# Performance work log

Measured on AMD Instinct MI355X. Metric: run time of the kernel, lower is better.

The kernel has to match this reference:

```python
import jax, jax.numpy as jnp
import numpy as np

DIM = 128
N = 4096


def setup_inputs() -> dict:
    key = jax.random.key(0)
    ks = jax.random.split(key, 12)
    d = DIM
    s = 0.02
    inp = jax.random.normal(ks[0], (N, 2 * d), dtype=jnp.float32)
    # H = myLinear: (2d -> 5d -> 1), tanh after each layer
    Hw1 = jax.random.normal(ks[1], (2 * d, 5 * d), dtype=jnp.float32) * s
    Hb1 = jax.random.normal(ks[2], (5 * d,), dtype=jnp.float32) * s
    Hw2 = jax.random.normal(ks[3], (5 * d, 1), dtype=jnp.float32) * s
    Hb2 = jax.random.normal(ks[4], (1,), dtype=jnp.float32) * s
    # augment_f: (d -> 4d -> 8d -> d*d), tanh after each layer
    Aw1 = jax.random.normal(ks[5], (d, 4 * d), dtype=jnp.float32) * s
    Ab1 = jax.random.normal(ks[6], (4 * d,), dtype=jnp.float32) * s
    Aw2 = jax.random.normal(ks[7], (4 * d, 8 * d), dtype=jnp.float32) * s
    Ab2 = jax.random.normal(ks[8], (8 * d,), dtype=jnp.float32) * s
    Aw3 = jax.random.normal(ks[9], (8 * d, d * d), dtype=jnp.float32) * s
    Ab3 = jax.random.normal(ks[10], (d * d,), dtype=jnp.float32) * s
    u = jax.random.uniform(ks[11], (d,), dtype=jnp.float32, minval=-0.001, maxval=0.001)
    return {"t": 0, "inp": inp, "Hw1": Hw1, "Hb1": Hb1, "Hw2": Hw2, "Hb2": Hb2,
            "Aw1": Aw1, "Ab1": Ab1, "Aw2": Aw2, "Ab2": Ab2, "Aw3": Aw3, "Ab3": Ab3, "u": u}


def reference(t, inp, Hw1, Hb1, Hw2, Hb2, Aw1, Ab1, Aw2, Ab2, Aw3, Ab3, u):
    d = DIM
    n = inp.shape[0]

    def H_scalar(z):  # z: [2d] -> scalar
        h = jnp.tanh(z @ Hw1 + Hb1)
        return jnp.tanh(h @ Hw2 + Hb2)[0]

    # per-sample gradient of scalar H w.r.t. input (== batch_jacobian squeeze)
    g = jax.vmap(jax.grad(H_scalar))(inp)  # [N, 2d]
    dx = g[:, :d]
    dv = -g[:, d:]

    x = inp[:, :d]
    h1 = jnp.tanh(x @ Aw1 + Ab1)            # [N, 4d]
    h2 = jnp.tanh(h1 @ Aw2 + Ab2)           # [N, 8d]
    gq = jnp.tanh(h2 @ Aw3 + Ab3).reshape(n, d, d)  # [N, d, d]
    dv = dv + jnp.einsum("nij,j->ni", gq, u)
    return jnp.concatenate([dx, dv], axis=-1)  # [N, 2d]
```

## Files before the change

### kernel.cpp

```cpp
#include <hip/hip_runtime.h>
#include <hip/hip_bf16.h>
#include <cstdint>


typedef __bf16 bf16_t;
typedef __bf16 bf16x4_t __attribute__((ext_vector_type(4)));
typedef __bf16 bf16x8_t __attribute__((ext_vector_type(8)));
typedef float f32x4_t __attribute__((ext_vector_type(4)));
typedef float f32x16_t __attribute__((ext_vector_type(16)));
typedef int intx4_t __attribute__((ext_vector_type(4)));
typedef int intx8_t __attribute__((ext_vector_type(8)));

#define DIMD 128
#define NROW 4096
#define SMEM_G64 24576
#define SMEM3_BYTES 24576

__device__ __forceinline__ float fast_tanh(float x) {
  float t = __builtin_amdgcn_exp2f(x * 2.8853900817779268f);
  return 1.f - 2.f * __builtin_amdgcn_rcpf(t + 1.f);
}

__device__ __forceinline__ uint8_t to_fp8(float x) {
  return (uint8_t)(__builtin_amdgcn_cvt_pk_fp8_f32(x, x, 0, false) & 0xff);
}

__device__ __forceinline__ uint32_t pk4_fp8(float a, float b, float c,
                                            float d) {
  uint32_t lo = (uint32_t)__builtin_amdgcn_cvt_pk_fp8_f32(a, b, 0, false);
  return (uint32_t)__builtin_amdgcn_cvt_pk_fp8_f32(c, d, lo, true);
}

__device__ __forceinline__ void g2l16(const void* gp, void* lp) {
  __builtin_amdgcn_global_load_lds(
      reinterpret_cast<__attribute__((address_space(1))) void*>(
          reinterpret_cast<uintptr_t>(gp)),
      reinterpret_cast<__attribute__((address_space(3))) void*>(
          reinterpret_cast<uintptr_t>(lp)),
      16, 0, 0);
}

template <int CTRL>
__device__ __forceinline__ float dpp_addf(float v) {
  return v + __int_as_float(__builtin_amdgcn_update_dpp(
                 0, __float_as_int(v), CTRL, 0xf, 0xf, true));
}
__device__ __forceinline__ float dpp_sum32(float v) {
  v = dpp_addf<0x111>(v);
  v = dpp_addf<0x112>(v);
  v = dpp_addf<0x114>(v);
  v = dpp_addf<0x118>(v);
  v = dpp_addf<0x142>(v);
  return v;
}

template <int EPI>
__device__ __forceinline__ void gemm64_body(char* smem, int bx, int by,
                                            const bf16_t* A, int lda,
                                            const bf16_t* B, int ldb, int K,
                                            const float* bias, void* outp,
                                            int ldo) {
  constexpr int BK = 32;
  bf16_t* As = (bf16_t*)smem;
  bf16_t* Bs = As + 3 * 2048;
  const int NT = K / BK;

  const int m0 = bx * 64;
  const int n0 = by * 64;
  const int tid = threadIdx.x;
  const int wave = tid >> 6;
  const int lane = tid & 63;
  const int wm = wave >> 1;
  const int wn = wave & 1;

  const int sr = lane >> 2;
  const int sk = (((lane & 3) ^ ((sr >> 1) & 3)) * 8);
  const int fr = lane & 15;
  const int fk = (((lane >> 4) ^ ((fr >> 1) & 3)) * 8);
  const int rb = wave * 16;

  const bf16_t* Ag = A + (size_t)(m0 + rb + sr) * lda + sk;
  const bf16_t* Bg = B + (size_t)(n0 + rb + sr) * ldb + sk;

#define G64_STAGE(buf, k0)                              \
  do {                                                  \
    g2l16(Ag + (k0), As + (buf) * 2048 + rb * BK);      \
    g2l16(Bg + (k0), Bs + (buf) * 2048 + rb * BK);      \
  } while (0)

  f32x4_t acc[2][2] = {};

  G64_STAGE(0, 0);
  G64_STAGE(1, BK);
  asm volatile("s_waitcnt vmcnt(2)" ::: "memory");
  __builtin_amdgcn_s_barrier();
  asm volatile("" ::: "memory");

  for (int t = 0; t < NT; ++t) {
    if (t + 2 < NT) G64_STAGE((t + 2) % 3, (t + 2) * BK);
    const bf16_t* Ab = As + (t % 3) * 2048;
    const bf16_t* Bb = Bs + (t % 3) * 2048;

    bf16x8_t af[2], bb[2];
#pragma unroll
    for (int u = 0; u < 2; ++u) {
      af[u] = *(const bf16x8_t*)(Ab + (wm * 32 + u * 16 + fr) * BK + fk);
      bb[u] = *(const bf16x8_t*)(Bb + (wn * 32 + u * 16 + fr) * BK + fk);
    }
#pragma unroll
    for (int i = 0; i < 2; ++i)
#pragma unroll
      for (int j = 0; j < 2; ++j)
        acc[i][j] = __builtin_amdgcn_mfma_f32_16x16x32_bf16(af[i], bb[j],
                                                            acc[i][j], 0, 0, 0);
    if (t < NT - 1) {
      if (t + 2 < NT)
        asm volatile("s_waitcnt vmcnt(2)" ::: "memory");
      else
        asm volatile("s_waitcnt vmcnt(0)" ::: "memory");
      __builtin_amdgcn_s_barrier();
      asm volatile("" ::: "memory");
    }
  }
#undef G64_STAGE

#pragma unroll
  for (int i = 0; i < 2; ++i) {
    const int row = m0 + wm * 32 + i * 16 + (lane >> 4) * 4;
#pragma unroll
    for (int j = 0; j < 2; ++j) {
      const int col = n0 + wn * 32 + j * 16 + fr;
      if constexpr (EPI == 0) {
        bf16_t* O = (bf16_t*)outp;
        const float b = bias[col];
#pragma unroll
        for (int r = 0; r < 4; ++r)
          O[(size_t)(row + r) * ldo + col] = (bf16_t)fast_tanh(acc[i][j][r] + b);
      } else {
        uint8_t* O = (uint8_t*)outp;
        const float b = bias[col];
        const int kb = col >> 6;
        const int khalf = (col >> 5) & 1;
        const int kin = col & 31;
#pragma unroll
        for (int r = 0; r < 4; ++r) {
          const int rw = row + r;
          O[(size_t)((rw >> 5) * 16 + kb) * 2048 +
            (khalf * 32 + (rw & 31)) * 32 + kin] =
              to_fp8(64.f * fast_tanh(acc[i][j][r] + b));
        }
      }
    }
  }
}

__device__ __forceinline__ void hbwd64_body(char* smem, int bx, int by,
                                            const bf16_t* A, int lda,
                                            const bf16_t* B, int ldb, int K,
                                            float* out, int ldo) {
  constexpr int BK = 32;
  bf16_t* As = (bf16_t*)smem;
  bf16_t* Bs = As + 3 * 2048;
  const int NT = K / BK;

  const int m0 = bx * 64;
  const int n0 = by * 64;
  const int tid = threadIdx.x;
  const int wave = tid >> 6;
  const int lane = tid & 63;
  const int wm = wave >> 2;
  const int wn = wave & 3;

  const int sr = lane >> 2;
  const int sk = (((lane & 3) ^ ((sr >> 1) & 3)) * 8);
  const int fr = lane & 15;
  const int fk = (((lane >> 4) ^ ((fr >> 1) & 3)) * 8);

  const int rbs = (wave & 3) * 16;
  const bf16_t* Sg = (wave < 4) ? A + (size_t)(m0 + rbs + sr) * lda + sk
                                : B + (size_t)(n0 + rbs + sr) * ldb + sk;
  bf16_t* Sl = ((wave < 4) ? As : Bs) + rbs * BK;

  f32x4_t acc[2] = {};

  g2l16(Sg, Sl);
  g2l16(Sg + BK, Sl + 2048);
  asm volatile("s_waitcnt vmcnt(1)" ::: "memory");
  __builtin_amdgcn_s_barrier();
  asm volatile("" ::: "memory");

  for (int t = 0; t < NT; ++t) {
    if (t + 2 < NT) g2l16(Sg + (t + 2) * BK, Sl + ((t + 2) % 3) * 2048);
    const bf16_t* Ab = As + (t % 3) * 2048;
    const bf16_t* Bb = Bs + (t % 3) * 2048;

    const bf16x8_t bb = *(const bf16x8_t*)(Bb + (wn * 16 + fr) * BK + fk);
#pragma unroll
    for (int u = 0; u < 2; ++u) {
      const bf16x8_t af =
          *(const bf16x8_t*)(Ab + (wm * 32 + u * 16 + fr) * BK + fk);
      acc[u] = __builtin_amdgcn_mfma_f32_16x16x32_bf16(af, bb, acc[u], 0, 0, 0);
    }
    if (t < NT - 1) {
      if (t + 2 < NT)
        asm volatile("s_waitcnt vmcnt(1)" ::: "memory");
      else
        asm volatile("s_waitcnt vmcnt(0)" ::: "memory");
      __builtin_amdgcn_s_barrier();
      asm volatile("" ::: "memory");
    }
  }

  const bool dx = (n0 < DIMD);
  const int col = n0 + wn * 16 + fr;
#pragma unroll
  for (int t = 0; t < 2; ++t) {
    const int row = m0 + wm * 32 + t * 16 + (lane >> 4) * 4;
#pragma unroll
    for (int r = 0; r < 4; ++r) {
      const size_t idx = (size_t)(row + r) * ldo + col;
      if (dx) out[idx] = acc[t][r];
      else atomicAdd(&out[idx], -acc[t][r]);
    }
  }
}

__device__ __forceinline__ void a3_body(int bx, int by, const uint8_t* AF,
                                        const uint8_t* BF, float* out,
                                        const float* ab3, const float* uvec) {
  const int tid = threadIdx.x;
  const int wave = tid >> 6;
  const int lane = tid & 63;
  const int wm = wave >> 1;
  const int wn = wave & 1;
  const int rl = lane & 31;
  const int m0 = bx * 256;
  const int n0 = by * 128;

  const uint8_t* bp[4];
#pragma unroll
  for (int i = 0; i < 2; ++i)
    bp[i] = AF + (size_t)(bx * 8 + wm * 2 + i) * 16 * 2048 + lane * 32;
#pragma unroll
  for (int j = 0; j < 2; ++j)
    bp[2 + j] = BF + (size_t)(by * 4 + wn * 2 + j) * 16 * 2048 + lane * 32;

  f32x16_t acc[2][2] = {};
  intx8_t s0[4], s1[4], s2[4];

#define A3_LD(S, koff)                                                       \
  _Pragma("unroll") for (int q = 0; q < 4; ++q) {                            \
    *(intx4_t*)&S[q] = *(const intx4_t*)(bp[q] + (koff)*2048);               \
    *((intx4_t*)&S[q] + 1) = *(const intx4_t*)(bp[q] + (koff)*2048 + 16);    \
  }

#define A3_MM(S)                                                             \
  acc[0][0] = __builtin_amdgcn_mfma_scale_f32_32x32x64_f8f6f4(               \
      S[0], S[2], acc[0][0], 0, 0, 0, 0x79797979, 0, 0x79797979);            \
  acc[0][1] = __builtin_amdgcn_mfma_scale_f32_32x32x64_f8f6f4(               \
      S[0], S[3], acc[0][1], 0, 0, 0, 0x79797979, 0, 0x79797979);            \
  acc[1][0] = __builtin_amdgcn_mfma_scale_f32_32x32x64_f8f6f4(               \
      S[1], S[2], acc[1][0], 0, 0, 0, 0x79797979, 0, 0x79797979);            \
  acc[1][1] = __builtin_amdgcn_mfma_scale_f32_32x32x64_f8f6f4(               \
      S[1], S[3], acc[1][1], 0, 0, 0, 0x79797979, 0, 0x79797979);

  A3_LD(s0, 0) A3_LD(s1, 1) A3_LD(s2, 2)
  A3_MM(s0) A3_LD(s0, 3)
  A3_MM(s1) A3_LD(s1, 4)
  A3_MM(s2) A3_LD(s2, 5)
  A3_MM(s0) A3_LD(s0, 6)
  A3_MM(s1) A3_LD(s1, 7)
  A3_MM(s2) A3_LD(s2, 8)
  A3_MM(s0) A3_LD(s0, 9)
  A3_MM(s1) A3_LD(s1, 10)
  A3_MM(s2) A3_LD(s2, 11)
  A3_MM(s0) A3_LD(s0, 12)
  A3_MM(s1) A3_LD(s1, 13)
  A3_MM(s2) A3_LD(s2, 14)
  A3_MM(s0) A3_LD(s0, 15)
  A3_MM(s1)
  A3_MM(s2)
  A3_MM(s0)
#undef A3_LD
#undef A3_MM

  const int q = lane >> 5;
  float uu[2], b3[2];
#pragma unroll
  for (int j = 0; j < 2; ++j) {
    uu[j] = uvec[wn * 64 + j * 32 + rl];
    b3[j] = ab3[n0 + wn * 64 + j * 32 + rl];
  }
  const int ocol = 128 + by;
#pragma unroll
  for (int i = 0; i < 2; ++i) {
    float s16[16];
#pragma unroll
    for (int r = 0; r < 16; ++r)
      s16[r] = fast_tanh(acc[i][0][r] + b3[0]) * uu[0] +
               fast_tanh(acc[i][1][r] + b3[1]) * uu[1];
#pragma unroll
    for (int r = 0; r < 16; ++r) s16[r] = dpp_sum32(s16[r]);
    if (rl == 31) {
      const int rowb = m0 + wm * 64 + i * 32 + 4 * q;
#pragma unroll
      for (int r = 0; r < 16; ++r)
        atomicAdd(&out[(size_t)(rowb + (r & 3) + 8 * (r >> 2)) * 256 + ocol],
                  s16[r]);
    }
  }
}

__device__ __forceinline__ void tcvt_body(char* smem, const float* in,
                                          bf16_t* out, int R, int C, int bx,
                                          int by) {
  float(*t)[33] = (float(*)[33])smem;
  const int c0 = bx * 32;
  const int r0 = by * 32;
  const int tx = threadIdx.x & 31;
  const int ty = threadIdx.x >> 5;
#pragma unroll
  for (int k = 0; k < 4; ++k)
    t[ty + k * 8][tx] = in[(size_t)(r0 + ty + k * 8) * C + c0 + tx];
  __syncthreads();
#pragma unroll
  for (int k = 0; k < 4; ++k)
    out[(size_t)(c0 + ty + k * 8) * R + r0 + tx] = (bf16_t)t[tx][ty + k * 8];
}

__device__ __forceinline__ void aw3t_body(char* smem, const float* Aw3,
                                          uint8_t* Aw3T8F, int b) {
  uint32_t(*T)[33] = (uint32_t(*)[33])smem;
  const int ct = b & 127;
  const int rt = b >> 7;
  const size_t c0 = (size_t)ct * 128;
  const int r0 = rt * 128;
  const int tx = threadIdx.x & 31;
  const int g = threadIdx.x >> 5;
#pragma unroll
  for (int k = 0; k < 4; ++k) {
    const int rr = r0 + 4 * g + 32 * k;
    const float4 v0 = *(const float4*)(Aw3 + (size_t)(rr + 0) * 16384 + c0 + 4 * tx);
    const float4 v1 = *(const float4*)(Aw3 + (size_t)(rr + 1) * 16384 + c0 + 4 * tx);
    const float4 v2 = *(const float4*)(Aw3 + (size_t)(rr + 2) * 16384 + c0 + 4 * tx);
    const float4 v3 = *(const float4*)(Aw3 + (size_t)(rr + 3) * 16384 + c0 + 4 * tx);
    const int r4 = g + 8 * k;
    T[4 * tx + 0][r4] = pk4_fp8(64.f * v0.x, 64.f * v1.x, 64.f * v2.x, 64.f * v3.x);
    T[4 * tx + 1][r4] = pk4_fp8(64.f * v0.y, 64.f * v1.y, 64.f * v2.y, 64.f * v3.y);
    T[4 * tx + 2][r4] = pk4_fp8(64.f * v0.z, 64.f * v1.z, 64.f * v2.z, 64.f * v3.z);
    T[4 * tx + 3][r4] = pk4_fp8(64.f * v0.w, 64.f * v1.w, 64.f * v2.w, 64.f * v3.w);
  }
  __syncthreads();
  const int kb = (rt << 1) + (tx >> 4);
  const int khalf = (tx >> 3) & 1;
  const int kin = (tx & 7) << 2;
#pragma unroll
  for (int k2 = 0; k2 < 16; ++k2) {
    const int cc = g + 8 * k2;
    const int cb = (ct << 2) + (cc >> 5);
    const int cin = cc & 31;
    *(uint32_t*)(Aw3T8F + (size_t)(cb * 16 + kb) * 2048 +
                 (khalf * 32 + cin) * 32 + kin) = T[cc][tx];
  }
}

__device__ __forceinline__ void hgrad_row(int row, const bf16_t* h,
                                          const float* Hw2, const float* Hb2,
                                          bf16_t* wout) {
  const int lane = threadIdx.x & 63;
  float hv[10], wv[10];
  float pre2 = 0.f;
#pragma unroll
  for (int t = 0; t < 10; ++t) {
    const int j = lane + t * 64;
    hv[t] = (float)h[(size_t)row * 640 + j];
    wv[t] = Hw2[j];
    pre2 += hv[t] * wv[t];
  }
#pragma unroll
  for (int d = 1; d < 64; d <<= 1) pre2 += __shfl_xor(pre2, d, 64);
  const float y = fast_tanh(pre2 + Hb2[0]);
  const float s = 1.f - y * y;
#pragma unroll
  for (int t = 0; t < 10; ++t) {
    const int j = lane + t * 64;
    wout[(size_t)row * 640 + j] = (bf16_t)(s * wv[t] * (1.f - hv[t] * hv[t]));
  }
}

__global__ __launch_bounds__(256) void launch0(
    const float* __restrict__ inp, bf16_t* __restrict__ inp_bf,
    const float* __restrict__ Hw1, bf16_t* __restrict__ Hw1T,
    bf16_t* __restrict__ Hw1_bf, const float* __restrict__ Aw1,
    bf16_t* __restrict__ Aw1T, const float* __restrict__ Aw2,
    bf16_t* __restrict__ Aw2T, float* __restrict__ out) {
  __shared__ __align__(16) char smem[4224];
  int b = blockIdx.x;
  if (b < 1024) {
    const int i = b * 256 + threadIdx.x;
    const float4 v = ((const float4*)inp)[i];
    bf16x4_t o = {(bf16_t)v.x, (bf16_t)v.y, (bf16_t)v.z, (bf16_t)v.w};
    ((bf16x4_t*)inp_bf)[i] = o;
  } else if (b < 1184) {
    int s = b - 1024;
    tcvt_body(smem, Hw1, Hw1T, 256, 640, s % 20, s / 20);
  } else if (b < 1248) {
    int s = b - 1184;
    tcvt_body(smem, Aw1, Aw1T, 128, 512, s % 16, s / 16);
  } else if (b < 1760) {
    int s = b - 1248;
    tcvt_body(smem, Aw2, Aw2T, 512, 1024, s % 32, s / 32);
  } else if (b < 1920) {
    const int i = (b - 1760) * 256 + threadIdx.x;
    const float4 v = ((const float4*)Hw1)[i];
    bf16x4_t o = {(bf16_t)v.x, (bf16_t)v.y, (bf16_t)v.z, (bf16_t)v.w};
    ((bf16x4_t*)Hw1_bf)[i] = o;
  } else {
    const int i = (b - 1920) * 256 + threadIdx.x;
    ((float4*)out)[i] = make_float4(0.f, 0.f, 0.f, 0.f);
  }
}

__global__ __launch_bounds__(256) void launch1(
    const bf16_t* __restrict__ inp_bf, const bf16_t* __restrict__ Hw1T,
    const float* __restrict__ Hb1, bf16_t* __restrict__ h_bf,
    const bf16_t* __restrict__ Aw1T, const float* __restrict__ Ab1,
    bf16_t* __restrict__ h1_bf, const float* __restrict__ Aw3,
    uint8_t* __restrict__ Aw3T8F) {
  __shared__ __align__(16) char smem[SMEM_G64];
  const int b = blockIdx.x;
  if (b < 640) {
    gemm64_body<0>(smem, b % 64, b / 64, inp_bf, 256, Hw1T, 256, 256, Hb1,
                   h_bf, 640);
  } else if (b < 1152) {
    const int i = b - 640;
    gemm64_body<0>(smem, i % 64, i / 64, inp_bf, 256, Aw1T, 128, 128, Ab1,
                   h1_bf, 512);
  } else {
    aw3t_body(smem, Aw3, Aw3T8F, b - 1152);
  }
}

__global__ __launch_bounds__(256) void launch2(
    const bf16_t* __restrict__ h1_bf, const bf16_t* __restrict__ Aw2T,
    const float* __restrict__ Ab2, uint8_t* __restrict__ h2F,
    const bf16_t* __restrict__ h_bf, const float* __restrict__ Hw2,
    const float* __restrict__ Hb2, bf16_t* __restrict__ w_bf,
    const float* __restrict__ Aw3, uint8_t* __restrict__ Aw3T8F) {
  __shared__ __align__(16) char smem[SMEM_G64];
  const int b = blockIdx.x;
  if (b < 1024) {
    gemm64_body<4>(smem, b % 64, b / 64, h1_bf, 512, Aw2T, 512, 512, Ab2,
                   h2F, 0);
  } else if (b < 2048) {
    const int row = (b - 1024) * 4 + (threadIdx.x >> 6);
    hgrad_row(row, h_bf, Hw2, Hb2, w_bf);
  } else {
    aw3t_body(smem, Aw3, Aw3T8F, 512 + (b - 2048));
  }
}

__global__ __launch_bounds__(512, 2) void launch3(
    const bf16_t* __restrict__ w_bf, const bf16_t* __restrict__ Hw1_bf,
    float* __restrict__ out, const uint8_t* __restrict__ h2F,
    const uint8_t* __restrict__ Aw3T8F, const float* __restrict__ Ab3,
    const float* __restrict__ uvec) {
  __shared__ __align__(16) char smem[SMEM3_BYTES];
  const int b = blockIdx.x;
  if (b < 256) {
    hbwd64_body(smem, b % 64, b / 64, w_bf, 640, Hw1_bf, 640, 640, out, 256);
  } else {
    const int p = b - 256;
    const int by = (p & 7) * 16 + ((p >> 3) & 15);
    const int bx = p >> 7;
    a3_body(bx, by, h2F, Aw3T8F, out, Ab3, uvec);
  }
}

extern "C" void kernel_launch(void* const* d_in, const int* in_sizes, int n_in,
                              void* d_out, int out_size, void* d_ws,
                              size_t ws_size, hipStream_t stream) {
  (void)in_sizes; (void)n_in; (void)out_size; (void)ws_size;
  const float* inp = (const float*)d_in[1];
  const float* Hw1 = (const float*)d_in[2];
  const float* Hb1 = (const float*)d_in[3];
  const float* Hw2 = (const float*)d_in[4];
  const float* Hb2 = (const float*)d_in[5];
  const float* Aw1 = (const float*)d_in[6];
  const float* Ab1 = (const float*)d_in[7];
  const float* Aw2 = (const float*)d_in[8];
  const float* Ab2 = (const float*)d_in[9];
  const float* Aw3 = (const float*)d_in[10];
  const float* Ab3 = (const float*)d_in[11];
  const float* u = (const float*)d_in[12];
  float* out = (float*)d_out;

  char* ws = (char*)d_ws;
  bf16_t* inp_bf = (bf16_t*)ws;    ws += (size_t)NROW * 256 * 2;
  bf16_t* Hw1_bf = (bf16_t*)ws;    ws += (size_t)256 * 640 * 2;
  bf16_t* Hw1T = (bf16_t*)ws;      ws += (size_t)640 * 256 * 2;
  bf16_t* Aw1T = (bf16_t*)ws;      ws += (size_t)512 * 128 * 2;
  bf16_t* Aw2T = (bf16_t*)ws;      ws += (size_t)1024 * 512 * 2;
  uint8_t* Aw3T8F = (uint8_t*)ws;  ws += (size_t)16384 * 1024;
  bf16_t* h_bf = (bf16_t*)ws;      ws += (size_t)NROW * 640 * 2;
  bf16_t* w_bf = (bf16_t*)ws;      ws += (size_t)NROW * 640 * 2;
  bf16_t* h1_bf = (bf16_t*)ws;     ws += (size_t)NROW * 512 * 2;
  uint8_t* h2F = (uint8_t*)ws;     ws += (size_t)NROW * 1024;

  launch0<<<2944, 256, 0, stream>>>(inp, inp_bf, Hw1, Hw1T, Hw1_bf, Aw1, Aw1T,
                                    Aw2, Aw2T, out);
  launch1<<<1664, 256, 0, stream>>>(inp_bf, Hw1T, Hb1, h_bf, Aw1T, Ab1, h1_bf,
                                    Aw3, Aw3T8F);
  launch2<<<2560, 256, 0, stream>>>(h1_bf, Aw2T, Ab2, h2F, h_bf, Hw2, Hb2,
                                    w_bf, Aw3, Aw3T8F);
  launch3<<<2304, 512, 0, stream>>>(w_bf, Hw1_bf, out, h2F, Aw3T8F, Ab3, u);
}
```

Measured before the change: 264.6 us.

## Shrink launch3 blocks to 256 threads and halve fp8 GEMM row tile

```diff
diff --git a/kernel.cpp b/kernel.cpp
--- a/kernel.cpp
+++ b/kernel.cpp
@@ -136,6 +136,15 @@
 #pragma unroll
         for (int r = 0; r < 4; ++r)
           O[(size_t)(row + r) * ldo + col] = (bf16_t)fast_tanh(acc[i][j][r] + b);
+      } else if constexpr (EPI == 1) {
+        float* O = (float*)outp;
+        const bool dx = (n0 < DIMD);
+#pragma unroll
+        for (int r = 0; r < 4; ++r) {
+          const size_t idx = (size_t)(row + r) * ldo + col;
+          if (dx) O[idx] = acc[i][j][r];
+          else atomicAdd(&O[idx], -acc[i][j][r]);
+        }
       } else {
         uint8_t* O = (uint8_t*)outp;
         const float b = bias[col];
@@ -150,77 +159,6 @@
               to_fp8(64.f * fast_tanh(acc[i][j][r] + b));
         }
       }
-    }
-  }
-}
-
-__device__ __forceinline__ void hbwd64_body(char* smem, int bx, int by,
-                                            const bf16_t* A, int lda,
-                                            const bf16_t* B, int ldb, int K,
-                                            float* out, int ldo) {
-  constexpr int BK = 32;
-  bf16_t* As = (bf16_t*)smem;
-  bf16_t* Bs = As + 3 * 2048;
-  const int NT = K / BK;
-
-  const int m0 = bx * 64;
-  const int n0 = by * 64;
-  const int tid = threadIdx.x;
-  const int wave = tid >> 6;
-  const int lane = tid & 63;
-  const int wm = wave >> 2;
-  const int wn = wave & 3;
-
-  const int sr = lane >> 2;
-  const int sk = (((lane & 3) ^ ((sr >> 1) & 3)) * 8);
-  const int fr = lane & 15;
-  const int fk = (((lane >> 4) ^ ((fr >> 1) & 3)) * 8);
-
-  const int rbs = (wave & 3) * 16;
-  const bf16_t* Sg = (wave < 4) ? A + (size_t)(m0 + rbs + sr) * lda + sk
-                                : B + (size_t)(n0 + rbs + sr) * ldb + sk;
-  bf16_t* Sl = ((wave < 4) ? As : Bs) + rbs * BK;
-
-  f32x4_t acc[2] = {};
-
-  g2l16(Sg, Sl);
-  g2l16(Sg + BK, Sl + 2048);
-  asm volatile("s_waitcnt vmcnt(1)" ::: "memory");
-  __builtin_amdgcn_s_barrier();
-  asm volatile("" ::: "memory");
-
-  for (int t = 0; t < NT; ++t) {
-    if (t + 2 < NT) g2l16(Sg + (t + 2) * BK, Sl + ((t + 2) % 3) * 2048);
-    const bf16_t* Ab = As + (t % 3) * 2048;
-    const bf16_t* Bb = Bs + (t % 3) * 2048;
-
-    const bf16x8_t bb = *(const bf16x8_t*)(Bb + (wn * 16 + fr) * BK + fk);
-#pragma unroll
-    for (int u = 0; u < 2; ++u) {
-      const bf16x8_t af =
-          *(const bf16x8_t*)(Ab + (wm * 32 + u * 16 + fr) * BK + fk);
-      acc[u] = __builtin_amdgcn_mfma_f32_16x16x32_bf16(af, bb, acc[u], 0, 0, 0);
-    }
-    if (t < NT - 1) {
-      if (t + 2 < NT)
-        asm volatile("s_waitcnt vmcnt(1)" ::: "memory");
-      else
-        asm volatile("s_waitcnt vmcnt(0)" ::: "memory");
-      __builtin_amdgcn_s_barrier();
-      asm volatile("" ::: "memory");
-    }
-  }
-
-  const bool dx = (n0 < DIMD);
-  const int col = n0 + wn * 16 + fr;
-#pragma unroll
-  for (int t = 0; t < 2; ++t) {
-    const int row = m0 + wm * 32 + t * 16 + (lane >> 4) * 4;
-#pragma unroll
-    for (int r = 0; r < 4; ++r) {
-      const size_t idx = (size_t)(row + r) * ldo + col;
-      if (dx) out[idx] = acc[t][r];
-      else atomicAdd(&out[idx], -acc[t][r]);
     }
   }
 }
@@ -234,13 +172,13 @@
   const int wm = wave >> 1;
   const int wn = wave & 1;
   const int rl = lane & 31;
-  const int m0 = bx * 256;
+  const int m0 = bx * 128;
   const int n0 = by * 128;
 
   const uint8_t* bp[4];
 #pragma unroll
   for (int i = 0; i < 2; ++i)
-    bp[i] = AF + (size_t)(bx * 8 + wm * 2 + i) * 16 * 2048 + lane * 32;
+    bp[i] = AF + (size_t)(bx * 4 + wm * 2 + i) * 16 * 2048 + lane * 32;
 #pragma unroll
   for (int j = 0; j < 2; ++j)
     bp[2 + j] = BF + (size_t)(by * 4 + wn * 2 + j) * 16 * 2048 + lane * 32;
@@ -460,7 +398,7 @@
   }
 }
 
-__global__ __launch_bounds__(512, 2) void launch3(
+__global__ __launch_bounds__(256, 3) void launch3(
     const bf16_t* __restrict__ w_bf, const bf16_t* __restrict__ Hw1_bf,
     float* __restrict__ out, const uint8_t* __restrict__ h2F,
     const uint8_t* __restrict__ Aw3T8F, const float* __restrict__ Ab3,
@@ -468,7 +406,8 @@
   __shared__ __align__(16) char smem[SMEM3_BYTES];
   const int b = blockIdx.x;
   if (b < 256) {
-    hbwd64_body(smem, b % 64, b / 64, w_bf, 640, Hw1_bf, 640, 640, out, 256);
+    gemm64_body<1>(smem, b % 64, b / 64, w_bf, 640, Hw1_bf, 640, 640, nullptr,
+                   out, 256);
   } else {
     const int p = b - 256;
     const int by = (p & 7) * 16 + ((p >> 3) & 15);
@@ -513,5 +452,5 @@
                                     Aw3, Aw3T8F);
   launch2<<<2560, 256, 0, stream>>>(h1_bf, Aw2T, Ab2, h2F, h_bf, Hw2, Hb2,
                                     w_bf, Aw3, Aw3T8F);
-  launch3<<<2304, 512, 0, stream>>>(w_bf, Hw1_bf, out, h2F, Aw3T8F, Ab3, u);
-}
+  launch3<<<4352, 256, 0, stream>>>(w_bf, Hw1_bf, out, h2F, Aw3T8F, Ab3, u);
+}
```

After: 240.6 us. 9.1% less time.
